# Optimization experiments

Measured on AMD Instinct MI355X. Metric: run time of the kernel, lower is better.

The kernel has to match this reference:

```python
import jax, jax.numpy as jnp
import numpy as np

B, H, W, C = 8, 128, 128, 256
NH, WS, SS = 8, 8, 4
MLP_H = 1024
N = WS * WS  # tokens per window


def _rel_pos_index(ws):
    coords = np.stack(np.meshgrid(np.arange(ws), np.arange(ws), indexing='ij'))  # (2, ws, ws)
    cf = coords.reshape(2, -1)
    rel = (cf[:, :, None] - cf[:, None, :]).transpose(1, 2, 0)  # (n, n, 2)
    rel[:, :, 0] += ws - 1
    rel[:, :, 1] += ws - 1
    rel[:, :, 0] *= 2 * ws - 1
    return rel.sum(-1).reshape(-1)  # (n*n,)


def _attn_mask(h, w, ws, ss):
    img = np.zeros((h, w))
    cnt = 0
    for hs in (slice(0, -ws), slice(-ws, -ss), slice(-ss, None)):
        for wsl in (slice(0, -ws), slice(-ws, -ss), slice(-ss, None)):
            img[hs, wsl] = cnt
            cnt += 1
    mw = img.reshape(h // ws, ws, w // ws, ws).transpose(0, 2, 1, 3).reshape(-1, ws * ws)
    am = mw[:, None, :] - mw[:, :, None]
    return np.where(am != 0, -100.0, 0.0).astype(np.float32)  # (nW, n, n)


_RPI = jnp.asarray(_rel_pos_index(WS))
_MASK = jnp.asarray(_attn_mask(H, W, WS, SS))


def _ln(x, g, b, eps=1e-5):
    mu = jnp.mean(x, -1, keepdims=True)
    var = jnp.mean(jnp.square(x - mu), -1, keepdims=True)
    return (x - mu) * jax.lax.rsqrt(var + eps) * g + b


def setup_inputs() -> dict:
    key = jax.random.key(0)
    ks = jax.random.split(key, 8)
    s = 0.02
    return {
        'x': jax.random.normal(ks[0], (B, H * W, C), jnp.float32),
        'g1': jnp.ones((C,), jnp.float32), 'b1': jnp.zeros((C,), jnp.float32),
        'qw': jax.random.normal(ks[1], (C, C), jnp.float32) * s,
        'qb': jnp.zeros((C,), jnp.float32),
        'kvw': jax.random.normal(ks[2], (C, 2 * C), jnp.float32) * s,
        'kvb': jnp.zeros((2 * C,), jnp.float32),
        'rpb': jax.random.normal(ks[3], ((2 * WS - 1) ** 2, NH), jnp.float32) * s,
        'projw': jax.random.normal(ks[4], (C, C), jnp.float32) * s,
        'projb': jnp.zeros((C,), jnp.float32),
        'g2': jnp.ones((C,), jnp.float32), 'b2': jnp.zeros((C,), jnp.float32),
        'fc1w': jax.random.normal(ks[5], (C, MLP_H), jnp.float32) * s,
        'fc1b': jnp.zeros((MLP_H,), jnp.float32),
        'fc2w': jax.random.normal(ks[6], (MLP_H, C), jnp.float32) * s,
        'fc2b': jnp.zeros((C,), jnp.float32),
    }


def reference(x, g1, b1, qw, qb, kvw, kvb, rpb, projw, projb, g2, b2, fc1w, fc1b, fc2w, fc2b):
    shortcut = x
    h = _ln(x, g1, b1).reshape(B, H, W, C)
    # cyclic shift for SW-MSA
    h = jnp.roll(h, (-SS, -SS), axis=(1, 2))
    # window partition -> (B*nW, N, C)
    hw = h.reshape(B, H // WS, WS, W // WS, WS, C).transpose(0, 1, 3, 2, 4, 5).reshape(-1, N, C)
    hd = C // NH
    q = (hw @ qw + qb).reshape(-1, N, NH, hd).transpose(0, 2, 1, 3)  # (bw, h, n, d)
    kv = (hw @ kvw + kvb).reshape(-1, N, 2, NH, hd).transpose(2, 0, 3, 1, 4)
    k, v = kv[0], kv[1]
    scale = hd ** (-0.5)
    attn = jnp.einsum('bhnd,bhmd->bhnm', q * scale, k)
    bias = rpb[_RPI].reshape(N, N, NH).transpose(2, 0, 1)  # (h, n, n)
    attn = attn + bias[None]
    nW = _MASK.shape[0]
    attn = attn.reshape(B, nW, NH, N, N) + _MASK[None, :, None]
    attn = jax.nn.softmax(attn.reshape(-1, NH, N, N), axis=-1)
    out = jnp.einsum('bhnm,bhmd->bhnd', attn, v).transpose(0, 2, 1, 3).reshape(-1, N, C)
    out = out @ projw + projb
    # window reverse + reverse shift
    out = out.reshape(B, H // WS, W // WS, WS, WS, C).transpose(0, 1, 3, 2, 4, 5).reshape(B, H, W, C)
    out = jnp.roll(out, (SS, SS), axis=(1, 2)).reshape(B, H * W, C)
    x = shortcut + out
    m = _ln(x, g2, b2)
    m = jax.nn.gelu(m @ fc1w + fc1b, approximate=False) @ fc2w + fc2b
    return x + m
```

## Files before the change

### kernel.cpp

```cpp
#include <hip/hip_runtime.h>
#include <hip/hip_bf16.h>


typedef __attribute__((ext_vector_type(8))) short bf16x8;
typedef __attribute__((ext_vector_type(4))) float f32x4;

#define QSCALE 0.17677669529663687f

__device__ __forceinline__ unsigned short f2bf(float f) {
  union { float f; unsigned u; } v; v.f = f;
  unsigned r = v.u + 0x7fffu + ((v.u >> 16) & 1u);
  return (unsigned short)(r >> 16);
}

__device__ __forceinline__ float gelu_f(float h) {
  const float t0 = h * h;
  const float y2 = h * fmaf(-0.0713548163f, t0, -1.5957691216f);
  const float e = __expf(y2);
  return h / (1.f + e);
}

__device__ __forceinline__ void gload_lds16(const unsigned short* g, void* l) {
  __builtin_amdgcn_global_load_lds(
      (const __attribute__((address_space(1))) unsigned int*)g,
      (__attribute__((address_space(3))) unsigned int*)l, 16, 0, 0);
}

__global__ __launch_bounds__(256) void wt_all(const float* __restrict__ qw,
                                              const float* __restrict__ kvw,
                                              const float* __restrict__ projw,
                                              const float* __restrict__ fc1w,
                                              const float* __restrict__ fc2w,
                                              unsigned short* __restrict__ dst) {
  const int e = blockIdx.x * 256 + threadIdx.x;
  float v;
  if (e < 65536) {
    const int n = e >> 8, k = e & 255;
    v = qw[k * 256 + n] * QSCALE;
  } else if (e < 196608) {
    const int l = e - 65536, n = l >> 8, k = l & 255;
    v = kvw[k * 512 + n];
  } else if (e < 262144) {
    const int l = e - 196608, n = l >> 8, k = l & 255;
    v = projw[k * 256 + n];
  } else if (e < 524288) {
    const int l = e - 262144, n = l >> 8, k = l & 255;
    v = fc1w[k * 1024 + n];
  } else {
    const int l = e - 524288, n = l >> 10, k = l & 1023;
    v = fc2w[k * 256 + n];
  }
  dst[e] = f2bf(v);
}

__global__ __launch_bounds__(256) void bias_tab(const float* __restrict__ rpb,
                                                float* __restrict__ tab) {
  const int e = blockIdx.x * 256 + threadIdx.x;
  const int type = e >> 15, rem = e & 32767;
  const int h = rem >> 12, nm = rem & 4095, n = nm >> 6, m = nm & 63;
  const int ni = n >> 3, nj = n & 7, mi = m >> 3, mj = m & 7;
  const float bias = rpb[((ni - mi + 7) * 15 + (nj - mj + 7)) * 8 + h];
  const int twi = type >> 1, twj = type & 1;
  const int rn = twi ? (ni < 4 ? 1 : 2) : 0;
  const int cn = twj ? (nj < 4 ? 1 : 2) : 0;
  const int rm_ = twi ? (mi < 4 ? 1 : 2) : 0;
  const int cm_ = twj ? (mj < 4 ? 1 : 2) : 0;
  tab[e] = bias + (((rn * 3 + cn) != (rm_ * 3 + cm_)) ? -100.f : 0.f);
}

__global__ __launch_bounds__(256) void ln1_win(const float* __restrict__ x,
                                               const float* __restrict__ g,
                                               const float* __restrict__ b,
                                               unsigned short* __restrict__ hw) {
  const int wv = threadIdx.x >> 6, ln = threadIdx.x & 63;
  const int r = blockIdx.x * 4 + wv;
  const int bw = r >> 6, n = r & 63;
  const int bb = bw >> 8, wi = (bw >> 4) & 15, wj = bw & 15;
  const int sh = (wi * 8 + (n >> 3) + 4) & 127;
  const int sw = (wj * 8 + (n & 7) + 4) & 127;
  const long src = ((long)bb * 16384 + sh * 128 + sw) * 256;
  float4 v = *(const float4*)(x + src + ln * 4);
  float s = v.x + v.y + v.z + v.w;
  float q = v.x * v.x + v.y * v.y + v.z * v.z + v.w * v.w;
#pragma unroll
  for (int m = 1; m < 64; m <<= 1) { s += __shfl_xor(s, m); q += __shfl_xor(q, m); }
  const float mu = s * (1.f / 256.f);
  const float rstd = rsqrtf(q * (1.f / 256.f) - mu * mu + 1e-5f);
  const int c = ln * 4;
  ushort4 o;
  o.x = f2bf((v.x - mu) * rstd * g[c + 0] + b[c + 0]);
  o.y = f2bf((v.y - mu) * rstd * g[c + 1] + b[c + 1]);
  o.z = f2bf((v.z - mu) * rstd * g[c + 2] + b[c + 2]);
  o.w = f2bf((v.w - mu) * rstd * g[c + 3] + b[c + 3]);
  *(ushort4*)(hw + (long)r * 256 + c) = o;
}

__global__ __launch_bounds__(256) void gemm_qkv(const unsigned short* __restrict__ A,
                                                const unsigned short* __restrict__ Bt,
                                                const float* __restrict__ qb,
                                                const float* __restrict__ kvb,
                                                unsigned short* __restrict__ out) {
  __shared__ char lds[32768];
  char* la = lds; char* lb = lds + 16384;
  const int tid = threadIdx.x, wv = tid >> 6, ln = tid & 63;
  const int lid = blockIdx.y * 6 + blockIdx.x;
  const int r8 = lid & 7, k6 = lid >> 3;
  const int tm = r8 * 128 + k6 / 6;
  const int tn = k6 - 6 * (k6 / 6);
  const long a_base = (long)tm * 128 * 256;
  const long b_base = (long)tn * 128 * 256;
  const int wr = (wv >> 1) * 64, wc = (wv & 1) * 64;
  f32x4 acc[4][4] = {};
  for (int ks = 0; ks < 4; ++ks) {
    const int k0 = ks * 64;
    __syncthreads();
#pragma unroll
    for (int it = 0; it < 4; ++it) {
      int d = wv * 4096 + it * 1024 + ln * 16;
      int row = d >> 7;
      int seg = ((d >> 4) & 7) ^ (row & 7);
      gload_lds16(A + a_base + row * 256 + k0 + seg * 8, la + wv * 4096 + it * 1024);
      gload_lds16(Bt + b_base + row * 256 + k0 + seg * 8, lb + wv * 4096 + it * 1024);
    }
    __syncthreads();
#pragma unroll
    for (int kk = 0; kk < 2; ++kk) {
      bf16x8 af[4], bfr[4];
      const int kb = (kk * 32 + (ln >> 4) * 8) * 2;
#pragma unroll
      for (int i = 0; i < 4; ++i) {
        int ra = wr + i * 16 + (ln & 15);
        af[i] = *(const bf16x8*)(la + ra * 128 + (kb ^ ((ra & 7) << 4)));
        int rb = wc + i * 16 + (ln & 15);
        bfr[i] = *(const bf16x8*)(lb + rb * 128 + (kb ^ ((rb & 7) << 4)));
      }
#pragma unroll
      for (int i = 0; i < 4; ++i)
#pragma unroll
        for (int j = 0; j < 4; ++j)
          acc[i][j] = __builtin_amdgcn_mfma_f32_16x16x32_bf16(af[i], bfr[j], acc[i][j], 0, 0, 0);
    }
  }
#pragma unroll
  for (int j = 0; j < 4; ++j) {
    const int col = tn * 128 + wc + j * 16 + (ln & 15);
    const float bias = (col < 256) ? qb[col] * QSCALE : kvb[col - 256];
#pragma unroll
    for (int i = 0; i < 4; ++i) {
      const int r0 = tm * 128 + wr + i * 16 + (ln >> 4) * 4;
#pragma unroll
      for (int rg = 0; rg < 4; ++rg)
        out[(long)(r0 + rg) * 768 + col] = f2bf(acc[i][j][rg] + bias);
    }
  }
}

__global__ __launch_bounds__(256, 2) void attn_proj(const unsigned short* __restrict__ qkv,
                                                    const float* __restrict__ tab,
                                                    const unsigned short* __restrict__ wp,
                                                    const float* __restrict__ pb,
                                                    const float* __restrict__ x,
                                                    float* __restrict__ x1) {
  __shared__ char lds[65536];
  const int tid = threadIdx.x, wv = tid >> 6, ln = tid & 63;
  const int bw = blockIdx.x;
  char* vt = lds + wv * 16384;
  char* pl = vt + 8192;
  const long base = (long)bw * 64 * 768;
#pragma unroll
  for (int it = 0; it < 8; ++it) {
    bf16x8 v = *(const bf16x8*)(qkv + base + (long)ln * 768 + 512 + wv * 64 + it * 8);
#pragma unroll
    for (int u = 0; u < 8; ++u) {
      const int d = it * 8 + u;
      *(unsigned short*)(vt + ((d * 128 + 2 * ln) ^ ((d & 7) << 4))) = (unsigned short)v[u];
    }
  }
  const int wi = (bw >> 4) & 15, wj = bw & 15;
  const int type = ((wi == 15) ? 2 : 0) | ((wj == 15) ? 1 : 0);
  f32x4 oo[2][4][2];
#pragma unroll
  for (int hh = 0; hh < 2; ++hh) {
    const int h = wv * 2 + hh;
    const float* Tb = tab + (((type << 3) + h) << 12) + (ln & 15);
    f32x4 s[4][4] = {};
    {
      bf16x8 qf[4], kf[4];
      const int dk = (ln >> 4) * 8;
#pragma unroll
      for (int i = 0; i < 4; ++i) {
        const long rq = base + (long)(i * 16 + (ln & 15)) * 768;
        qf[i] = *(const bf16x8*)(qkv + rq + h * 32 + dk);
        kf[i] = *(const bf16x8*)(qkv + rq + 256 + h * 32 + dk);
      }
#pragma unroll
      for (int i = 0; i < 4; ++i)
#pragma unroll
        for (int j = 0; j < 4; ++j)
          s[i][j] = __builtin_amdgcn_mfma_f32_16x16x32_bf16(qf[i], kf[j], s[i][j], 0, 0, 0);
    }
#pragma unroll
    for (int i = 0; i < 4; ++i)
#pragma unroll
      for (int rg = 0; rg < 4; ++rg) {
        const int n = i * 16 + (ln >> 4) * 4 + rg;
        const float* Tn = Tb + n * 64;
#pragma unroll
        for (int j = 0; j < 4; ++j)
          s[i][j][rg] += Tn[j * 16];
      }
#pragma unroll
    for (int i = 0; i < 4; ++i)
#pragma unroll
      for (int rg = 0; rg < 4; ++rg) {
        float mx = fmaxf(fmaxf(s[i][0][rg], s[i][1][rg]), fmaxf(s[i][2][rg], s[i][3][rg]));
        mx = fmaxf(mx, __shfl_xor(mx, 1));
        mx = fmaxf(mx, __shfl_xor(mx, 2));
        mx = fmaxf(mx, __shfl_xor(mx, 4));
        mx = fmaxf(mx, __shfl_xor(mx, 8));
        float sum = 0.f;
#pragma unroll
        for (int j = 0; j < 4; ++j) { float e = __expf(s[i][j][rg] - mx); s[i][j][rg] = e; sum += e; }
        sum += __shfl_xor(sum, 1);
        sum += __shfl_xor(sum, 2);
        sum += __shfl_xor(sum, 4);
        sum += __shfl_xor(sum, 8);
        const float inv = 1.f / sum;
#pragma unroll
        for (int j = 0; j < 4; ++j) s[i][j][rg] *= inv;
      }
#pragma unroll
    for (int i = 0; i < 4; ++i)
#pragma unroll
      for (int rg = 0; rg < 4; ++rg) {
        const int n = i * 16 + (ln >> 4) * 4 + rg;
#pragma unroll
        for (int j = 0; j < 4; ++j) {
          const int m = j * 16 + (ln & 15);
          *(unsigned short*)(pl + n * 128 + ((m * 2) ^ ((n & 7) << 4))) = f2bf(s[i][j][rg]);
        }
      }
#pragma unroll
    for (int i = 0; i < 4; ++i)
#pragma unroll
      for (int j = 0; j < 2; ++j) oo[hh][i][j] = (f32x4){0.f, 0.f, 0.f, 0.f};
#pragma unroll
    for (int kk = 0; kk < 2; ++kk) {
      const int km = kk * 32 + (ln >> 4) * 8;
      bf16x8 pa[4], vb[2];
#pragma unroll
      for (int i = 0; i < 4; ++i) {
        const int n = i * 16 + (ln & 15);
        pa[i] = *(const bf16x8*)(pl + n * 128 + ((km * 2) ^ ((n & 7) << 4)));
      }
#pragma unroll
      for (int j = 0; j < 2; ++j) {
        const int r = hh * 32 + j * 16 + (ln & 15);
        vb[j] = *(const bf16x8*)(vt + ((r * 128 + km * 2) ^ ((r & 7) << 4)));
      }
#pragma unroll
      for (int i = 0; i < 4; ++i)
#pragma unroll
        for (int j = 0; j < 2; ++j)
          oo[hh][i][j] = __builtin_amdgcn_mfma_f32_16x16x32_bf16(pa[i], vb[j], oo[hh][i][j], 0, 0, 0);
    }
  }
  __syncthreads();
#pragma unroll
  for (int hh = 0; hh < 2; ++hh)
#pragma unroll
    for (int i = 0; i < 4; ++i)
#pragma unroll
      for (int j = 0; j < 2; ++j)
#pragma unroll
        for (int rg = 0; rg < 4; ++rg) {
          const int t = i * 16 + (ln >> 4) * 4 + rg;
          const int c = wv * 64 + hh * 32 + j * 16 + (ln & 15);
          *(unsigned short*)(lds + t * 512 + ((c * 2) ^ ((t & 7) << 4))) = f2bf(oo[hh][i][j][rg]);
        }
  __syncthreads();
  f32x4 acc[4][4] = {};
#pragma unroll
  for (int kk = 0; kk < 8; ++kk) {
    bf16x8 af[4], bfr[4];
    const int kb = (kk * 32 + (ln >> 4) * 8) * 2;
#pragma unroll
    for (int i = 0; i < 4; ++i) {
      const int ra = i * 16 + (ln & 15);
      af[i] = *(const bf16x8*)(lds + ra * 512 + (kb ^ ((ra & 7) << 4)));
    }
#pragma unroll
    for (int j = 0; j < 4; ++j)
      bfr[j] = *(const bf16x8*)(wp + (long)(wv * 64 + j * 16 + (ln & 15)) * 256 +
                                kk * 32 + (ln >> 4) * 8);
#pragma unroll
    for (int i = 0; i < 4; ++i)
#pragma unroll
      for (int j = 0; j < 4; ++j)
        acc[i][j] = __builtin_amdgcn_mfma_f32_16x16x32_bf16(af[i], bfr[j], acc[i][j], 0, 0, 0);
  }
  const int bb = bw >> 8;
#pragma unroll
  for (int i = 0; i < 4; ++i)
#pragma unroll
    for (int rg = 0; rg < 4; ++rg) {
      const int n = i * 16 + (ln >> 4) * 4 + rg;
      const int sh = (wi * 8 + (n >> 3) + 4) & 127;
      const int sw = (wj * 8 + (n & 7) + 4) & 127;
      const long dst = ((long)bb * 16384 + sh * 128 + sw) * 256;
#pragma unroll
      for (int j = 0; j < 4; ++j) {
        const int col = wv * 64 + j * 16 + (ln & 15);
        x1[dst + col] = x[dst + col] + acc[i][j][rg] + pb[col];
      }
    }
}

__global__ __launch_bounds__(256, 2) void mlp_fused(const float* __restrict__ x1,
                                                    const float* __restrict__ g2,
                                                    const float* __restrict__ b2,
                                                    const unsigned short* __restrict__ w1t,
                                                    const float* __restrict__ fb1,
                                                    const unsigned short* __restrict__ w2t,
                                                    const float* __restrict__ fb2,
                                                    float* __restrict__ out) {
  __shared__ char lds[65536];
  char* h0 = lds + 32768;
  char* h1 = lds + 49152;
  const int tid = threadIdx.x, wv = tid >> 6, ln = tid & 63;
  const long rbase = (long)blockIdx.x * 64;
  {
    const int t = tid >> 2, q = tid & 3;
    const float* xr = x1 + (rbase + t) * 256 + q * 64;
    float4 v[16];
    float s = 0.f, sq = 0.f;
#pragma unroll
    for (int u = 0; u < 16; ++u) {
      v[u] = *(const float4*)(xr + u * 4);
      s += v[u].x + v[u].y + v[u].z + v[u].w;
      sq += v[u].x * v[u].x + v[u].y * v[u].y + v[u].z * v[u].z + v[u].w * v[u].w;
    }
    s += __shfl_xor(s, 1); s += __shfl_xor(s, 2);
    sq += __shfl_xor(sq, 1); sq += __shfl_xor(sq, 2);
    const float mu = s * (1.f / 256.f);
    const float rstd = rsqrtf(sq * (1.f / 256.f) - mu * mu + 1e-5f);
#pragma unroll
    for (int c8 = 0; c8 < 8; ++c8) {
      bf16x8 o;
#pragma unroll
      for (int u = 0; u < 8; ++u) {
        const int col = q * 64 + c8 * 8 + u;
        const float fv = ((&v[c8 * 2 + (u >> 2)].x)[u & 3] - mu) * rstd * g2[col] + b2[col];
        o[u] = (short)f2bf(fv);
      }
      *(bf16x8*)(lds + t * 512 + (((q * 64 + c8 * 8) * 2) ^ ((t & 7) << 4))) = o;
    }
  }

  f32x4 acc[4][4] = {};
  f32x4 hc[4][2];

  auto fc1_compute = [&](int ch) {
#pragma unroll
    for (int i = 0; i < 4; ++i)
#pragma unroll
      for (int j = 0; j < 2; ++j) hc[i][j] = (f32x4){0.f, 0.f, 0.f, 0.f};
#pragma unroll
    for (int ks = 0; ks < 8; ++ks) {
      bf16x8 af[4], wf[2];
#pragma unroll
      for (int j = 0; j < 2; ++j)
        wf[j] = *(const bf16x8*)(w1t + (long)(ch * 128 + wv * 32 + j * 16 + (ln & 15)) * 256 +
                                 ks * 32 + (ln >> 4) * 8);
      const int kb = (ks * 32 + (ln >> 4) * 8) * 2;
#pragma unroll
      for (int i = 0; i < 4; ++i) {
        const int ra = i * 16 + (ln & 15);
        af[i] = *(const bf16x8*)(lds + ra * 512 + (kb ^ ((ra & 7) << 4)));
      }
#pragma unroll
      for (int i = 0; i < 4; ++i)
#pragma unroll
        for (int j = 0; j < 2; ++j)
          hc[i][j] = __builtin_amdgcn_mfma_f32_16x16x32_bf16(af[i], wf[j], hc[i][j], 0, 0, 0);
    }
  };

  auto gelu_store = [&](int ch, char* hdst) {
#pragma unroll
    for (int j = 0; j < 2; ++j) {
      const int cH = wv * 32 + j * 16 + (ln & 15);
      const float fb = fb1[ch * 128 + cH];
#pragma unroll
      for (int i = 0; i < 4; ++i)
#pragma unroll
        for (int rg = 0; rg < 4; ++rg) {
          const int t = i * 16 + (ln >> 4) * 4 + rg;
          const float val = hc[i][j][rg] + fb;
          *(unsigned short*)(hdst + t * 256 + ((cH * 2) ^ ((t & 7) << 4))) = f2bf(gelu_f(val));
        }
    }
  };

  auto fc2_compute = [&](int ch, const char* hsrc) {
#pragma unroll
    for (int kk = 0; kk < 4; ++kk) {
      const int kb2 = kk * 32 + (ln >> 4) * 8;
      bf16x8 ha[4], wb[4];
#pragma unroll
      for (int j = 0; j < 4; ++j)
        wb[j] = *(const bf16x8*)(w2t + (long)(wv * 64 + j * 16 + (ln & 15)) * 1024 +
                                 ch * 128 + kb2);
#pragma unroll
      for (int i = 0; i < 4; ++i) {
        const int tt = i * 16 + (ln & 15);
        ha[i] = *(const bf16x8*)(hsrc + tt * 256 + ((kb2 * 2) ^ ((tt & 7) << 4)));
      }
#pragma unroll
      for (int i = 0; i < 4; ++i)
#pragma unroll
        for (int j = 0; j < 4; ++j)
          acc[i][j] = __builtin_amdgcn_mfma_f32_16x16x32_bf16(ha[i], wb[j], acc[i][j], 0, 0, 0);
    }
  };

  __syncthreads();
  fc1_compute(0);
  gelu_store(0, h0);
  __syncthreads();
#pragma unroll 2
  for (int ch = 0; ch < 8; ++ch) {
    char* hr = (ch & 1) ? h1 : h0;
    char* hw2 = (ch & 1) ? h0 : h1;
    if (ch < 7) fc1_compute(ch + 1);
    fc2_compute(ch, hr);
    if (ch < 7) {
      gelu_store(ch + 1, hw2);
      __syncthreads();
    }
  }
#pragma unroll
  for (int i = 0; i < 4; ++i)
#pragma unroll
    for (int rg = 0; rg < 4; ++rg) {
      const long t = rbase + i * 16 + (ln >> 4) * 4 + rg;
#pragma unroll
      for (int j = 0; j < 4; ++j) {
        const int col = wv * 64 + j * 16 + (ln & 15);
        out[t * 256 + col] = x1[t * 256 + col] + acc[i][j][rg] + fb2[col];
      }
    }
}

extern "C" void kernel_launch(void* const* d_in, const int* in_sizes, int n_in,
                              void* d_out, int out_size, void* d_ws, size_t ws_size,
                              hipStream_t stream) {
  const float* x     = (const float*)d_in[0];
  const float* g1    = (const float*)d_in[1];
  const float* b1    = (const float*)d_in[2];
  const float* qw    = (const float*)d_in[3];
  const float* qb    = (const float*)d_in[4];
  const float* kvw   = (const float*)d_in[5];
  const float* kvb   = (const float*)d_in[6];
  const float* rpb   = (const float*)d_in[7];
  const float* projw = (const float*)d_in[8];
  const float* projb = (const float*)d_in[9];
  const float* g2    = (const float*)d_in[10];
  const float* b2    = (const float*)d_in[11];
  const float* fc1w  = (const float*)d_in[12];
  const float* fc1b  = (const float*)d_in[13];
  const float* fc2w  = (const float*)d_in[14];
  const float* fc2b  = (const float*)d_in[15];

  unsigned short* wqkv  = (unsigned short*)d_ws;
  unsigned short* wproj = wqkv + 196608;
  unsigned short* wfc1  = wproj + 65536;
  unsigned short* wfc2  = wfc1 + 262144;
  unsigned short* qkv   = wfc2 + 262144;
  float* tab = (float*)(qkv + 100663296);
  unsigned short* hw = (unsigned short*)d_out;
  float* x1 = (float*)d_out;

  wt_all<<<3072, 256, 0, stream>>>(qw, kvw, projw, fc1w, fc2w, wqkv);
  bias_tab<<<512, 256, 0, stream>>>(rpb, tab);

  ln1_win<<<32768, 256, 0, stream>>>(x, g1, b1, hw);
  gemm_qkv<<<dim3(6, 1024), 256, 0, stream>>>(hw, wqkv, qb, kvb, qkv);
  attn_proj<<<2048, 256, 0, stream>>>(qkv, tab, wproj, projb, x, x1);
  mlp_fused<<<2048, 256, 0, stream>>>(x1, g2, b2, wfc1, fc1b, wfc2, fc2b,
                                      (float*)d_out);
}
```

Measured before the change: 633.3 us.

## Split fused MLP into LN2 kernel plus tiled FC1 and FC2 GEMMs

Replaces the single fused LN2+FC1+GELU+FC2 kernel, which streamed weights from global memory per 64-row block, with three kernels. A standalone LN2 writes bf16 activations, then LDS-tiled 128x128 GEMMs compute FC1 with GELU into a global hidden buffer and FC2 with the residual add. The work runs in two halves so the hidden buffer fits in the workspace. This gains better weight reuse through LDS tiling, but it costs an extra round trip of the 4x-wide hidden activations through HBM and more kernel launches.

```diff
diff --git a/kernel.cpp b/kernel.cpp
--- a/kernel.cpp
+++ b/kernel.cpp
@@ -95,6 +95,28 @@
   *(ushort4*)(hw + (long)r * 256 + c) = o;
 }
 
+__global__ __launch_bounds__(256) void ln2_tok(const float* __restrict__ x1,
+                                               const float* __restrict__ g,
+                                               const float* __restrict__ b,
+                                               unsigned short* __restrict__ aln) {
+  const int wv = threadIdx.x >> 6, ln = threadIdx.x & 63;
+  const long r = (long)blockIdx.x * 4 + wv;
+  float4 v = *(const float4*)(x1 + r * 256 + ln * 4);
+  float s = v.x + v.y + v.z + v.w;
+  float q = v.x * v.x + v.y * v.y + v.z * v.z + v.w * v.w;
+#pragma unroll
+  for (int m = 1; m < 64; m <<= 1) { s += __shfl_xor(s, m); q += __shfl_xor(q, m); }
+  const float mu = s * (1.f / 256.f);
+  const float rstd = rsqrtf(q * (1.f / 256.f) - mu * mu + 1e-5f);
+  const int c = ln * 4;
+  ushort4 o;
+  o.x = f2bf((v.x - mu) * rstd * g[c + 0] + b[c + 0]);
+  o.y = f2bf((v.y - mu) * rstd * g[c + 1] + b[c + 1]);
+  o.z = f2bf((v.z - mu) * rstd * g[c + 2] + b[c + 2]);
+  o.w = f2bf((v.w - mu) * rstd * g[c + 3] + b[c + 3]);
+  *(ushort4*)(aln + r * 256 + c) = o;
+}
+
 __global__ __launch_bounds__(256) void gemm_qkv(const unsigned short* __restrict__ A,
                                                 const unsigned short* __restrict__ Bt,
                                                 const float* __restrict__ qb,
@@ -155,6 +177,127 @@
   }
 }
 
+__global__ __launch_bounds__(256) void gemm_fc1(const unsigned short* __restrict__ A,
+                                                const unsigned short* __restrict__ Bt,
+                                                const float* __restrict__ fb1,
+                                                unsigned short* __restrict__ H) {
+  __shared__ char lds[32768];
+  char* la = lds; char* lb = lds + 16384;
+  const int tid = threadIdx.x, wv = tid >> 6, ln = tid & 63;
+  const int lid = blockIdx.y * 8 + blockIdx.x;
+  const int r8 = lid & 7, k8 = lid >> 3;
+  const int tm = r8 * 64 + (k8 >> 3);
+  const int tn = k8 & 7;
+  const long a_base = (long)tm * 128 * 256;
+  const long b_base = (long)tn * 128 * 256;
+  const int wr = (wv >> 1) * 64, wc = (wv & 1) * 64;
+  f32x4 acc[4][4] = {};
+  for (int ks = 0; ks < 4; ++ks) {
+    const int k0 = ks * 64;
+    __syncthreads();
+#pragma unroll
+    for (int it = 0; it < 4; ++it) {
+      int d = wv * 4096 + it * 1024 + ln * 16;
+      int row = d >> 7;
+      int seg = ((d >> 4) & 7) ^ (row & 7);
+      gload_lds16(A + a_base + row * 256 + k0 + seg * 8, la + wv * 4096 + it * 1024);
+      gload_lds16(Bt + b_base + row * 256 + k0 + seg * 8, lb + wv * 4096 + it * 1024);
+    }
+    __syncthreads();
+#pragma unroll
+    for (int kk = 0; kk < 2; ++kk) {
+      bf16x8 af[4], bfr[4];
+      const int kb = (kk * 32 + (ln >> 4) * 8) * 2;
+#pragma unroll
+      for (int i = 0; i < 4; ++i) {
+        int ra = wr + i * 16 + (ln & 15);
+        af[i] = *(const bf16x8*)(la + ra * 128 + (kb ^ ((ra & 7) << 4)));
+        int rb = wc + i * 16 + (ln & 15);
+        bfr[i] = *(const bf16x8*)(lb + rb * 128 + (kb ^ ((rb & 7) << 4)));
+      }
+#pragma unroll
+      for (int i = 0; i < 4; ++i)
+#pragma unroll
+        for (int j = 0; j < 4; ++j)
+          acc[i][j] = __builtin_amdgcn_mfma_f32_16x16x32_bf16(af[i], bfr[j], acc[i][j], 0, 0, 0);
+    }
+  }
+#pragma unroll
+  for (int j = 0; j < 4; ++j) {
+    const int col = tn * 128 + wc + j * 16 + (ln & 15);
+    const float fb = fb1[col];
+#pragma unroll
+    for (int i = 0; i < 4; ++i) {
+      const int r0 = tm * 128 + wr + i * 16 + (ln >> 4) * 4;
+#pragma unroll
+      for (int rg = 0; rg < 4; ++rg)
+        H[(long)(r0 + rg) * 1024 + col] = f2bf(gelu_f(acc[i][j][rg] + fb));
+    }
+  }
+}
+
+__global__ __launch_bounds__(256) void gemm_fc2(const unsigned short* __restrict__ A,
+                                                const unsigned short* __restrict__ Bt,
+                                                const float* __restrict__ fb2,
+                                                const float* __restrict__ x1,
+                                                float* __restrict__ out,
+                                                int mbase) {
+  __shared__ char lds[32768];
+  char* la = lds; char* lb = lds + 16384;
+  const int tid = threadIdx.x, wv = tid >> 6, ln = tid & 63;
+  const int lid = blockIdx.y * 2 + blockIdx.x;
+  const int r8 = lid & 7, k2 = lid >> 3;
+  const int tm = r8 * 64 + (k2 >> 1);
+  const int tn = k2 & 1;
+  const long a_base = (long)tm * 128 * 1024;
+  const long b_base = (long)tn * 128 * 1024;
+  const int wr = (wv >> 1) * 64, wc = (wv & 1) * 64;
+  f32x4 acc[4][4] = {};
+  for (int ks = 0; ks < 16; ++ks) {
+    const int k0 = ks * 64;
+    __syncthreads();
+#pragma unroll
+    for (int it = 0; it < 4; ++it) {
+      int d = wv * 4096 + it * 1024 + ln * 16;
+      int row = d >> 7;
+      int seg = ((d >> 4) & 7) ^ (row & 7);
+      gload_lds16(A + a_base + row * 1024 + k0 + seg * 8, la + wv * 4096 + it * 1024);
+      gload_lds16(Bt + b_base + row * 1024 + k0 + seg * 8, lb + wv * 4096 + it * 1024);
+    }
+    __syncthreads();
+#pragma unroll
+    for (int kk = 0; kk < 2; ++kk) {
+      bf16x8 af[4], bfr[4];
+      const int kb = (kk * 32 + (ln >> 4) * 8) * 2;
+#pragma unroll
+      for (int i = 0; i < 4; ++i) {
+        int ra = wr + i * 16 + (ln & 15);
+        af[i] = *(const bf16x8*)(la + ra * 128 + (kb ^ ((ra & 7) << 4)));
+        int rb = wc + i * 16 + (ln & 15);
+        bfr[i] = *(const bf16x8*)(lb + rb * 128 + (kb ^ ((rb & 7) << 4)));
+      }
+#pragma unroll
+      for (int i = 0; i < 4; ++i)
+#pragma unroll
+        for (int j = 0; j < 4; ++j)
+          acc[i][j] = __builtin_amdgcn_mfma_f32_16x16x32_bf16(af[i], bfr[j], acc[i][j], 0, 0, 0);
+    }
+  }
+#pragma unroll
+  for (int i = 0; i < 4; ++i) {
+    const int r0 = tm * 128 + wr + i * 16 + (ln >> 4) * 4;
+#pragma unroll
+    for (int rg = 0; rg < 4; ++rg) {
+      const long R = (long)mbase + r0 + rg;
+#pragma unroll
+      for (int j = 0; j < 4; ++j) {
+        const int col = tn * 128 + wc + j * 16 + (ln & 15);
+        out[R * 256 + col] = x1[R * 256 + col] + acc[i][j][rg] + fb2[col];
+      }
+    }
+  }
+}
+
 __global__ __launch_bounds__(256, 2) void attn_proj(const unsigned short* __restrict__ qkv,
                                                     const float* __restrict__ tab,
                                                     const unsigned short* __restrict__ wp,
@@ -312,142 +455,6 @@
       for (int j = 0; j < 4; ++j) {
         const int col = wv * 64 + j * 16 + (ln & 15);
         x1[dst + col] = x[dst + col] + acc[i][j][rg] + pb[col];
-      }
-    }
-}
-
-__global__ __launch_bounds__(256, 2) void mlp_fused(const float* __restrict__ x1,
-                                                    const float* __restrict__ g2,
-                                                    const float* __restrict__ b2,
-                                                    const unsigned short* __restrict__ w1t,
-                                                    const float* __restrict__ fb1,
-                                                    const unsigned short* __restrict__ w2t,
-                                                    const float* __restrict__ fb2,
-                                                    float* __restrict__ out) {
-  __shared__ char lds[65536];
-  char* h0 = lds + 32768;
-  char* h1 = lds + 49152;
-  const int tid = threadIdx.x, wv = tid >> 6, ln = tid & 63;
-  const long rbase = (long)blockIdx.x * 64;
-  {
-    const int t = tid >> 2, q = tid & 3;
-    const float* xr = x1 + (rbase + t) * 256 + q * 64;
-    float4 v[16];
-    float s = 0.f, sq = 0.f;
-#pragma unroll
-    for (int u = 0; u < 16; ++u) {
-      v[u] = *(const float4*)(xr + u * 4);
-      s += v[u].x + v[u].y + v[u].z + v[u].w;
-      sq += v[u].x * v[u].x + v[u].y * v[u].y + v[u].z * v[u].z + v[u].w * v[u].w;
-    }
-    s += __shfl_xor(s, 1); s += __shfl_xor(s, 2);
-    sq += __shfl_xor(sq, 1); sq += __shfl_xor(sq, 2);
-    const float mu = s * (1.f / 256.f);
-    const float rstd = rsqrtf(sq * (1.f / 256.f) - mu * mu + 1e-5f);
-#pragma unroll
-    for (int c8 = 0; c8 < 8; ++c8) {
-      bf16x8 o;
-#pragma unroll
-      for (int u = 0; u < 8; ++u) {
-        const int col = q * 64 + c8 * 8 + u;
-        const float fv = ((&v[c8 * 2 + (u >> 2)].x)[u & 3] - mu) * rstd * g2[col] + b2[col];
-        o[u] = (short)f2bf(fv);
-      }
-      *(bf16x8*)(lds + t * 512 + (((q * 64 + c8 * 8) * 2) ^ ((t & 7) << 4))) = o;
-    }
-  }
-
-  f32x4 acc[4][4] = {};
-  f32x4 hc[4][2];
-
-  auto fc1_compute = [&](int ch) {
-#pragma unroll
-    for (int i = 0; i < 4; ++i)
-#pragma unroll
-      for (int j = 0; j < 2; ++j) hc[i][j] = (f32x4){0.f, 0.f, 0.f, 0.f};
-#pragma unroll
-    for (int ks = 0; ks < 8; ++ks) {
-      bf16x8 af[4], wf[2];
-#pragma unroll
-      for (int j = 0; j < 2; ++j)
-        wf[j] = *(const bf16x8*)(w1t + (long)(ch * 128 + wv * 32 + j * 16 + (ln & 15)) * 256 +
-                                 ks * 32 + (ln >> 4) * 8);
-      const int kb = (ks * 32 + (ln >> 4) * 8) * 2;
-#pragma unroll
-      for (int i = 0; i < 4; ++i) {
-        const int ra = i * 16 + (ln & 15);
-        af[i] = *(const bf16x8*)(lds + ra * 512 + (kb ^ ((ra & 7) << 4)));
-      }
-#pragma unroll
-      for (int i = 0; i < 4; ++i)
-#pragma unroll
-        for (int j = 0; j < 2; ++j)
-          hc[i][j] = __builtin_amdgcn_mfma_f32_16x16x32_bf16(af[i], wf[j], hc[i][j], 0, 0, 0);
-    }
-  };
-
-  auto gelu_store = [&](int ch, char* hdst) {
-#pragma unroll
-    for (int j = 0; j < 2; ++j) {
-      const int cH = wv * 32 + j * 16 + (ln & 15);
-      const float fb = fb1[ch * 128 + cH];
-#pragma unroll
-      for (int i = 0; i < 4; ++i)
-#pragma unroll
-        for (int rg = 0; rg < 4; ++rg) {
-          const int t = i * 16 + (ln >> 4) * 4 + rg;
-          const float val = hc[i][j][rg] + fb;
-          *(unsigned short*)(hdst + t * 256 + ((cH * 2) ^ ((t & 7) << 4))) = f2bf(gelu_f(val));
-        }
-    }
-  };
-
-  auto fc2_compute = [&](int ch, const char* hsrc) {
-#pragma unroll
-    for (int kk = 0; kk < 4; ++kk) {
-      const int kb2 = kk * 32 + (ln >> 4) * 8;
-      bf16x8 ha[4], wb[4];
-#pragma unroll
-      for (int j = 0; j < 4; ++j)
-        wb[j] = *(const bf16x8*)(w2t + (long)(wv * 64 + j * 16 + (ln & 15)) * 1024 +
-                                 ch * 128 + kb2);
-#pragma unroll
-      for (int i = 0; i < 4; ++i) {
-        const int tt = i * 16 + (ln & 15);
-        ha[i] = *(const bf16x8*)(hsrc + tt * 256 + ((kb2 * 2) ^ ((tt & 7) << 4)));
-      }
-#pragma unroll
-      for (int i = 0; i < 4; ++i)
-#pragma unroll
-        for (int j = 0; j < 4; ++j)
-          acc[i][j] = __builtin_amdgcn_mfma_f32_16x16x32_bf16(ha[i], wb[j], acc[i][j], 0, 0, 0);
-    }
-  };
-
-  __syncthreads();
-  fc1_compute(0);
-  gelu_store(0, h0);
-  __syncthreads();
-#pragma unroll 2
-  for (int ch = 0; ch < 8; ++ch) {
-    char* hr = (ch & 1) ? h1 : h0;
-    char* hw2 = (ch & 1) ? h0 : h1;
-    if (ch < 7) fc1_compute(ch + 1);
-    fc2_compute(ch, hr);
-    if (ch < 7) {
-      gelu_store(ch + 1, hw2);
-      __syncthreads();
-    }
-  }
-#pragma unroll
-  for (int i = 0; i < 4; ++i)
-#pragma unroll
-    for (int rg = 0; rg < 4; ++rg) {
-      const long t = rbase + i * 16 + (ln >> 4) * 4 + rg;
-#pragma unroll
-      for (int j = 0; j < 4; ++j) {
-        const int col = wv * 64 + j * 16 + (ln & 15);
-        out[t * 256 + col] = x1[t * 256 + col] + acc[i][j][rg] + fb2[col];
       }
     }
 }
@@ -477,6 +484,8 @@
   unsigned short* wfc1  = wproj + 65536;
   unsigned short* wfc2  = wfc1 + 262144;
   unsigned short* qkv   = wfc2 + 262144;
+  unsigned short* aln   = qkv;
+  unsigned short* Hbuf  = qkv + 33554432;
   float* tab = (float*)(qkv + 100663296);
   unsigned short* hw = (unsigned short*)d_out;
   float* x1 = (float*)d_out;
@@ -487,6 +496,9 @@
   ln1_win<<<32768, 256, 0, stream>>>(x, g1, b1, hw);
   gemm_qkv<<<dim3(6, 1024), 256, 0, stream>>>(hw, wqkv, qb, kvb, qkv);
   attn_proj<<<2048, 256, 0, stream>>>(qkv, tab, wproj, projb, x, x1);
-  mlp_fused<<<2048, 256, 0, stream>>>(x1, g2, b2, wfc1, fc1b, wfc2, fc2b,
-                                      (float*)d_out);
-}
+  ln2_tok<<<32768, 256, 0, stream>>>(x1, g2, b2, aln);
+  gemm_fc1<<<dim3(8, 512), 256, 0, stream>>>(aln, wfc1, fc1b, Hbuf);
+  gemm_fc2<<<dim3(2, 512), 256, 0, stream>>>(Hbuf, wfc2, fc2b, x1, (float*)d_out, 0);
+  gemm_fc1<<<dim3(8, 512), 256, 0, stream>>>(aln + (long)65536 * 256, wfc1, fc1b, Hbuf);
+  gemm_fc2<<<dim3(2, 512), 256, 0, stream>>>(Hbuf, wfc2, fc2b, x1, (float*)d_out, 65536);
+}
```

After: 693.8 us. +9.5%, slower.
